# Kernel tuning notes

Hardware: AMD Instinct MI355X
Metric: run time of the kernel (lower is better)

The kernel has to match this reference:

```python
import jax, jax.numpy as jnp
import numpy as np

HEIGHT = 108
WIDTH = 108
LEN_CLASSES = 7
EPS = 1e-5


def layout_bbox(pred, H, W):
    # pred: [B, O, 4 + LEN_CLASSES]
    bbox = pred[..., :4]
    cls_prob = pred[..., 4:]  # [B,O,7]
    x_c = bbox[..., 0] * W   # [B,O]
    y_c = bbox[..., 1] * H
    w = bbox[..., 2] * W
    h = bbox[..., 3] * H
    x1 = (x_c - 0.5 * w)[:, :, None, None]  # [B,O,1,1]
    x2 = (x_c + 0.5 * w)[:, :, None, None]
    y1 = (y_c - 0.5 * h)[:, :, None, None]
    y2 = (y_c + 0.5 * h)[:, :, None, None]
    xt = jnp.arange(W, dtype=pred.dtype)[None, None, None, :]  # [1,1,1,W]
    yt = jnp.arange(H, dtype=pred.dtype)[None, None, :, None]  # [1,1,H,1]
    x1d = xt - x1  # [B,O,1,W]
    x2d = x2 - xt
    y1d = yt - y1  # [B,O,H,1]
    y2d = y2 - yt
    # min(relu(d), 1) == clip(d, 0, 1)
    yband = jnp.clip(y1d, 0.0, 1.0) * jnp.clip(y2d, 0.0, 1.0)  # [B,O,H,1]
    xband = jnp.clip(x1d, 0.0, 1.0) * jnp.clip(x2d, 0.0, 1.0)  # [B,O,1,W]
    x1_line = jax.nn.relu(1.0 - jnp.abs(x1d)) * yband  # [B,O,H,W]
    x2_line = jax.nn.relu(1.0 - jnp.abs(x2d)) * yband
    y1_line = jax.nn.relu(1.0 - jnp.abs(y1d)) * xband
    y2_line = jax.nn.relu(1.0 - jnp.abs(y2d)) * xband
    xy_max = jnp.maximum(jnp.maximum(x1_line, x2_line), jnp.maximum(y1_line, y2_line))  # [B,O,H,W]
    spatial = xy_max[..., None] * cls_prob[:, :, None, None, :]  # [B,O,H,W,7]
    return jnp.max(spatial, axis=1)  # [B,H,W,7]


def bn(x, g, b, axes):
    m = jnp.mean(x, axis=axes, keepdims=True)
    v = jnp.var(x, axis=axes, keepdims=True)
    shape = [1] * x.ndim
    shape[1 if x.ndim == 4 else -1] = -1
    return (x - m) * jax.lax.rsqrt(v + EPS) * g.reshape(shape) + b.reshape(shape)


def conv2d(x, w, b, stride):
    y = jax.lax.conv_general_dilated(x, w, (stride, stride), 'VALID',
                                     dimension_numbers=('NCHW', 'OIHW', 'NCHW'))
    return y + b[None, :, None, None]


def setup_inputs() -> dict:
    key = jax.random.key(0)
    ks = jax.random.split(key, 16)
    B, O = 64, 16
    d = {}
    d['image'] = jax.random.uniform(ks[0], (B, O, 4 + LEN_CLASSES), dtype=jnp.float32)
    d['conv1_w'] = jax.random.normal(ks[1], (32, LEN_CLASSES, 5, 5), jnp.float32) * 0.05
    d['conv1_b'] = jnp.zeros((32,), jnp.float32)
    d['bn1_g'] = jnp.ones((32,), jnp.float32)
    d['bn1_b'] = jnp.zeros((32,), jnp.float32)
    d['conv2_w'] = jax.random.normal(ks[2], (64, 32, 5, 5), jnp.float32) * 0.03
    d['conv2_b'] = jnp.zeros((64,), jnp.float32)
    d['bn2_g'] = jnp.ones((64,), jnp.float32)
    d['bn2_b'] = jnp.zeros((64,), jnp.float32)
    d['fc1_w'] = jax.random.normal(ks[3], (512, 36864), jnp.float32) * 0.005
    d['fc1_b'] = jnp.zeros((512,), jnp.float32)
    d['bn3_g'] = jnp.ones((512,), jnp.float32)
    d['bn3_b'] = jnp.zeros((512,), jnp.float32)
    d['fc2_w'] = jax.random.normal(ks[4], (1, 512), jnp.float32) * 0.04
    d['fc2_b'] = jnp.zeros((1,), jnp.float32)
    return d


def reference(image, conv1_w, conv1_b, bn1_g, bn1_b, conv2_w, conv2_b, bn2_g, bn2_b,
              fc1_w, fc1_b, bn3_g, bn3_b, fc2_w, fc2_b):
    # layout_bbox(image, WIDTH, HEIGHT): output_height=WIDTH, output_width=HEIGHT (both 108)
    layout = layout_bbox(image, WIDTH, HEIGHT)           # [B,108,108,7]
    x = jnp.transpose(layout, (0, 3, 1, 2))              # [B,7,108,108]
    x = conv2d(x, conv1_w, conv1_b, 2)                   # [B,32,52,52]
    x = bn(x, bn1_g, bn1_b, (0, 2, 3))
    x = jax.nn.leaky_relu(x, 0.2)
    x = conv2d(x, conv2_w, conv2_b, 2)                   # [B,64,24,24]
    x = bn(x, bn2_g, bn2_b, (0, 2, 3))
    x = jax.nn.leaky_relu(x, 0.2)
    x = x.reshape(x.shape[0], -1)                        # [B,36864]
    x = x @ fc1_w.T + fc1_b                              # [B,512]
    x = bn(x, bn3_g, bn3_b, (0,))
    x = jax.nn.leaky_relu(x, 0.2)
    x = x @ fc2_w.T + fc2_b                              # [B,1]
    return jax.nn.sigmoid(x)
```

## Files before the change

### kernel.cpp

```cpp
#include <hip/hip_runtime.h>
#include <hip/hip_bf16.h>


typedef unsigned short u16;
typedef __attribute__((ext_vector_type(8))) short bf8_t;
typedef __attribute__((ext_vector_type(4))) float f4_t;
#define MFMA16(a, b, c) __builtin_amdgcn_mfma_f32_16x16x32_bf16(a, b, c, 0, 0, 0)

#define LEAKY(v) (fmaxf((v), 0.2f * (v)))
#define CLIP01(v) fminf(fmaxf((v), 0.0f), 1.0f)

__device__ inline unsigned f2bf(float f) {
  unsigned u = __float_as_uint(f);
  return (u + 0x7FFFu + ((u >> 16) & 1u)) >> 16;
}
__device__ inline float bf2f(unsigned u) { return __uint_as_float(u << 16); }

constexpr int HW = 108;
constexpr int NOBJ = 16;
constexpr int NCLS = 7;

__global__ __launch_bounds__(128) void layout_prep_kernel(
    const float* __restrict__ image, const float* __restrict__ w1,
    const float* __restrict__ w2, u16* __restrict__ lay8,
    u16* __restrict__ wB1, u16* __restrict__ wB2, float* __restrict__ st) {
  int h = blockIdx.x, b = blockIdx.y;
  int tid = threadIdx.x;
  int bid = b * 108 + h;
  if (bid < 114) {
#pragma unroll
    for (int j = 0; j < 4; ++j) {
      int i = bid * 512 + j * 128 + tid;
      if (i < 1216) st[i] = 0.f;
      if (i < 7168) {
        int co = i / 224, k = i % 224;
        int chunk = k >> 5, kk = k & 31, tl = kk >> 3, ci = kk & 7;
        int tap = chunk * 4 + tl;
        unsigned v = 0;
        if (tap < 25 && ci < 7) v = f2bf(w1[co * 175 + ci * 25 + tap]);
        wB1[i] = (u16)v;
      } else if (i < 58368) {
        int jj = i - 7168;
        int tap = jj / 2048, r = jj % 2048, co = r >> 5, ci = r & 31;
        wB2[jj] = (u16)f2bf(w2[co * 800 + ci * 25 + tap]);
      }
    }
  }
  __shared__ float sIm[NOBJ * 11];
  for (int i = tid; i < NOBJ * 11; i += 128) sIm[i] = image[b * NOBJ * 11 + i];
  __syncthreads();
  int w = tid;
  if (w >= HW) return;
  float best[NCLS];
#pragma unroll
  for (int c = 0; c < NCLS; ++c) best[c] = 0.0f;
  float fw = (float)w, fh = (float)h;
  for (int o = 0; o < NOBJ; ++o) {
    const float* p = &sIm[o * 11];
    float xc = p[0] * 108.0f, yc = p[1] * 108.0f;
    float wd = p[2] * 108.0f, hd = p[3] * 108.0f;
    float x1 = xc - 0.5f * wd, x2 = xc + 0.5f * wd;
    float y1 = yc - 0.5f * hd, y2 = yc + 0.5f * hd;
    float x1d = fw - x1, x2d = x2 - fw;
    float y1d = fh - y1, y2d = y2 - fh;
    float yband = CLIP01(y1d) * CLIP01(y2d);
    float xband = CLIP01(x1d) * CLIP01(x2d);
    float x1l = fmaxf(1.0f - fabsf(x1d), 0.0f) * yband;
    float x2l = fmaxf(1.0f - fabsf(x2d), 0.0f) * yband;
    float y1l = fmaxf(1.0f - fabsf(y1d), 0.0f) * xband;
    float y2l = fmaxf(1.0f - fabsf(y2d), 0.0f) * xband;
    float xy = fmaxf(fmaxf(x1l, x2l), fmaxf(y1l, y2l));
#pragma unroll
    for (int c = 0; c < NCLS; ++c) best[c] = fmaxf(best[c], xy * p[4 + c]);
  }
  unsigned p0 = f2bf(best[0]) | (f2bf(best[1]) << 16);
  unsigned p1 = f2bf(best[2]) | (f2bf(best[3]) << 16);
  unsigned p2 = f2bf(best[4]) | (f2bf(best[5]) << 16);
  unsigned p3 = f2bf(best[6]);
  uint4 stv = {p0, p1, p2, p3};
  ((uint4*)lay8)[b * 11664 + h * 108 + w] = stv;
}

__global__ __launch_bounds__(128) void conv1_mfma(
    const u16* __restrict__ lay8, const u16* __restrict__ wB1,
    u16* __restrict__ x1r, float* __restrict__ bn1sum,
    float* __restrict__ bn1sq) {
  int mtg = blockIdx.x, nt = blockIdx.y, bz = blockIdx.z;
  int tid = threadIdx.x;
  int lane = tid & 63, wv = tid >> 6;
  int f = lane & 15, q = lane >> 4;
  int co = nt * 16 + f;
  int b0 = bz * 4 + wv * 2;
  int pbase[4];
  bool mvalid[4];
#pragma unroll
  for (int t = 0; t < 4; ++t) {
    int mt = mtg * 4 + t;
    mvalid[t] = mt < 169;
    int P = min(mt * 16 + f, 2703);
    int oh = P / 52, ow = P - oh * 52;
    pbase[t] = (oh * 2 * 108 + ow * 2) * 8;
  }
  f4_t acc[2][4];
#pragma unroll
  for (int b2 = 0; b2 < 2; ++b2)
#pragma unroll
    for (int t = 0; t < 4; ++t) acc[b2][t] = {0.f, 0.f, 0.f, 0.f};
#pragma unroll
  for (int chunk = 0; chunk < 7; ++chunk) {
    int tap = chunk * 4 + q;
    tap = tap > 24 ? 24 : tap;
    int kh = tap / 5, kw = tap - kh * 5;
    int toff = (kh * 108 + kw) * 8;
    bf8_t bf = *(const bf8_t*)&wB1[co * 224 + chunk * 32 + q * 8];
#pragma unroll
    for (int b2 = 0; b2 < 2; ++b2) {
      const u16* lb = lay8 + (size_t)(b0 + b2) * 93312;
#pragma unroll
      for (int t = 0; t < 4; ++t) {
        bf8_t af = *(const bf8_t*)&lb[pbase[t] + toff];
        acc[b2][t] = MFMA16(af, bf, acc[b2][t]);
      }
    }
  }
  float s = 0.f, sq = 0.f;
#pragma unroll
  for (int b2 = 0; b2 < 2; ++b2) {
    u16* ob = x1r + (size_t)(b0 + b2) * 86528;
#pragma unroll
    for (int t = 0; t < 4; ++t) {
      if (!mvalid[t]) continue;
      int P0 = (mtg * 4 + t) * 16 + q * 4;
#pragma unroll
      for (int r = 0; r < 4; ++r) {
        float v = acc[b2][t][r];
        s += v;
        sq += v * v;
        ob[(P0 + r) * 32 + co] = (u16)f2bf(v);
      }
    }
  }
  s += __shfl_xor(s, 16);
  s += __shfl_xor(s, 32);
  sq += __shfl_xor(sq, 16);
  sq += __shfl_xor(sq, 32);
  __shared__ float rs[2][16], rq[2][16];
  if (lane < 16) {
    rs[wv][f] = s;
    rq[wv][f] = sq;
  }
  __syncthreads();
  if (tid < 16) {
    atomicAdd(&bn1sum[nt * 16 + tid], rs[0][tid] + rs[1][tid]);
    atomicAdd(&bn1sq[nt * 16 + tid], rq[0][tid] + rq[1][tid]);
  }
}

__global__ __launch_bounds__(256) void bnapply1_kernel(
    const u16* __restrict__ x1r, const float* __restrict__ bn1sum,
    const float* __restrict__ bn1sq, const float* __restrict__ g1,
    const float* __restrict__ b1, u16* __restrict__ x1b) {
  int idx = blockIdx.x * 256 + threadIdx.x;
  int base = idx * 8, c0 = base & 31;
  float sc[8], sh[8];
#pragma unroll
  for (int j = 0; j < 8; ++j) {
    int c = c0 + j;
    float mean = bn1sum[c] * (1.f / 173056.f);
    float var = bn1sq[c] * (1.f / 173056.f) - mean * mean;
    float s = g1[c] * rsqrtf(var + 1e-5f);
    sc[j] = s;
    sh[j] = b1[c] - mean * s;
  }
  uint4 in = *(const uint4*)&x1r[base];
  unsigned w[4] = {in.x, in.y, in.z, in.w};
  unsigned out[4];
#pragma unroll
  for (int j = 0; j < 4; ++j) {
    float a = bf2f(w[j] & 0xffffu);
    float bq = bf2f(w[j] >> 16);
    a = LEAKY(fmaf(a, sc[2 * j], sh[2 * j]));
    bq = LEAKY(fmaf(bq, sc[2 * j + 1], sh[2 * j + 1]));
    out[j] = f2bf(a) | (f2bf(bq) << 16);
  }
  uint4 stv = {out[0], out[1], out[2], out[3]};
  *(uint4*)&x1b[base] = stv;
}

__global__ __launch_bounds__(256) void conv2_mfma(
    const u16* __restrict__ x1b, const u16* __restrict__ wB2,
    u16* __restrict__ x2b, float* __restrict__ bn2sum,
    float* __restrict__ bn2sq) {
  int mt = blockIdx.x, ntg = blockIdx.y, bz = blockIdx.z;
  int tid = threadIdx.x;
  int lane = tid & 63, wv = tid >> 6;
  int f = lane & 15, q = lane >> 4;
  int co0 = ntg * 32;
  int b0 = bz * 16 + wv * 4;
  int P = mt * 16 + f;
  int oh = P / 24, ow = P - oh * 24;
  int abase = (oh * 2 * 52 + ow * 2) * 32 + q * 8;
  f4_t acc[4][2];
#pragma unroll
  for (int b2 = 0; b2 < 4; ++b2)
#pragma unroll
    for (int n = 0; n < 2; ++n) acc[b2][n] = {0.f, 0.f, 0.f, 0.f};
#pragma unroll
  for (int tap = 0; tap < 25; ++tap) {
    int kh = tap / 5, kw = tap - kh * 5;
    int toff = (kh * 52 + kw) * 32;
    bf8_t bf0 = *(const bf8_t*)&wB2[tap * 2048 + (co0 + f) * 32 + q * 8];
    bf8_t bf1 = *(const bf8_t*)&wB2[tap * 2048 + (co0 + 16 + f) * 32 + q * 8];
#pragma unroll
    for (int b2 = 0; b2 < 4; ++b2) {
      bf8_t af =
          *(const bf8_t*)&x1b[(size_t)(b0 + b2) * 86528 + abase + toff];
      acc[b2][0] = MFMA16(af, bf0, acc[b2][0]);
      acc[b2][1] = MFMA16(af, bf1, acc[b2][1]);
    }
  }
  float s[2] = {0.f, 0.f}, sq[2] = {0.f, 0.f};
#pragma unroll
  for (int b2 = 0; b2 < 4; ++b2) {
    u16* ob = x2b + (size_t)(b0 + b2) * 36864;
#pragma unroll
    for (int n = 0; n < 2; ++n)
#pragma unroll
      for (int r = 0; r < 4; ++r) {
        float v = acc[b2][n][r];
        s[n] += v;
        sq[n] += v * v;
        ob[(mt * 16 + q * 4 + r) * 64 + co0 + n * 16 + f] = (u16)f2bf(v);
      }
  }
#pragma unroll
  for (int n = 0; n < 2; ++n) {
    s[n] += __shfl_xor(s[n], 16);
    s[n] += __shfl_xor(s[n], 32);
    sq[n] += __shfl_xor(sq[n], 16);
    sq[n] += __shfl_xor(sq[n], 32);
  }
  __shared__ float rs[4][32], rq[4][32];
  if (lane < 16) {
#pragma unroll
    for (int n = 0; n < 2; ++n) {
      rs[wv][n * 16 + f] = s[n];
      rq[wv][n * 16 + f] = sq[n];
    }
  }
  __syncthreads();
  if (tid < 32) {
    atomicAdd(&bn2sum[co0 + tid],
              rs[0][tid] + rs[1][tid] + rs[2][tid] + rs[3][tid]);
    atomicAdd(&bn2sq[co0 + tid],
              rq[0][tid] + rq[1][tid] + rq[2][tid] + rq[3][tid]);
  }
}

__global__ __launch_bounds__(256) void bnapply2t_kernel(
    const u16* __restrict__ x2b, const float* __restrict__ bn2sum,
    const float* __restrict__ bn2sq, const float* __restrict__ g2,
    const float* __restrict__ b2, u16* __restrict__ xB) {
  int hw0 = blockIdx.x * 64, b = blockIdx.y;
  __shared__ float tile[64 * 65];
  int t = threadIdx.x;
  int c = t & 63, hl4 = t >> 6;
  float mean = bn2sum[c] * (1.f / 36864.f);
  float var = bn2sq[c] * (1.f / 36864.f) - mean * mean;
  float s = g2[c] * rsqrtf(var + 1e-5f);
  float h = b2[c] - mean * s;
#pragma unroll
  for (int it = 0; it < 16; ++it) {
    int hl = it * 4 + hl4;
    float v = bf2f((unsigned)x2b[((size_t)b * 576 + hw0 + hl) * 64 + c]);
    tile[hl * 65 + c] = LEAKY(fmaf(v, s, h));
  }
  __syncthreads();
  int hw = t & 63, cl4 = t >> 6;
#pragma unroll
  for (int it = 0; it < 16; ++it) {
    int cc = it * 4 + cl4;
    xB[(size_t)b * 36864 + cc * 576 + hw0 + hw] = (u16)f2bf(tile[hw * 65 + cc]);
  }
}

__global__ __launch_bounds__(256) void fc1_mfma(
    const u16* __restrict__ xB, const float* __restrict__ wgt,
    float* __restrict__ part) {
  int ks = blockIdx.x, nb = blockIdx.y;
  int tid = threadIdx.x;
  int lane = tid & 63, wv = tid >> 6;
  int f = lane & 15, q = lane >> 4;
  int n0 = nb * 64 + wv * 16;
  int kbase = ks * 512;
  __shared__ u16 sA[64 * 520];
#pragma unroll
  for (int i = 0; i < 16; ++i) {
    int c = i * 256 + tid;
    int row = c >> 6, col = c & 63;
    *(uint4*)&sA[row * 520 + col * 8] =
        *(const uint4*)&xB[(size_t)row * 36864 + kbase + col * 8];
  }
  __syncthreads();
  f4_t acc[4];
#pragma unroll
  for (int m = 0; m < 4; ++m) acc[m] = {0.f, 0.f, 0.f, 0.f};
  const float* wrow = wgt + (size_t)(n0 + f) * 36864 + kbase + q * 8;
#pragma unroll 4
  for (int kt = 0; kt < 16; ++kt) {
    const float* wp = wrow + kt * 32;
    float4 wa = *(const float4*)wp;
    float4 wb = *(const float4*)(wp + 4);
    union { bf8_t v; u16 u[8]; } bu;
    bu.u[0] = (u16)f2bf(wa.x); bu.u[1] = (u16)f2bf(wa.y);
    bu.u[2] = (u16)f2bf(wa.z); bu.u[3] = (u16)f2bf(wa.w);
    bu.u[4] = (u16)f2bf(wb.x); bu.u[5] = (u16)f2bf(wb.y);
    bu.u[6] = (u16)f2bf(wb.z); bu.u[7] = (u16)f2bf(wb.w);
    bf8_t afr[4];
#pragma unroll
    for (int m = 0; m < 4; ++m)
      afr[m] = *(const bf8_t*)&sA[(m * 16 + f) * 520 + kt * 32 + q * 8];
#pragma unroll
    for (int m = 0; m < 4; ++m) acc[m] = MFMA16(afr[m], bu.v, acc[m]);
  }
  float* pp = part + (size_t)ks * 32768;
#pragma unroll
  for (int m = 0; m < 4; ++m)
#pragma unroll
    for (int r = 0; r < 4; ++r)
      pp[(m * 16 + q * 4 + r) * 512 + n0 + f] = acc[m][r];
}

__global__ __launch_bounds__(256) void fc1_reduce_kernel(
    const float* __restrict__ part, float* __restrict__ fc1o,
    float* __restrict__ bn3sum, float* __restrict__ bn3sq) {
  int i = blockIdx.x * 256 + threadIdx.x;
  float s = 0.f;
#pragma unroll 8
  for (int ks = 0; ks < 72; ++ks) s += part[(size_t)ks * 32768 + i];
  fc1o[i] = s;
  atomicAdd(&bn3sum[i & 511], s);
  atomicAdd(&bn3sq[i & 511], s * s);
}

__global__ __launch_bounds__(64) void fc2_kernel(
    const float* __restrict__ fc1o, const float* __restrict__ bn3sum,
    const float* __restrict__ bn3sq, const float* __restrict__ g3,
    const float* __restrict__ b3, const float* __restrict__ w2,
    const float* __restrict__ b2o, float* __restrict__ out) {
  int m = blockIdx.x;
  int fl = threadIdx.x;
  float a = 0.f;
#pragma unroll
  for (int j = 0; j < 8; ++j) {
    int ff = fl + j * 64;
    float mean = bn3sum[ff] * (1.f / 64.f);
    float var = bn3sq[ff] * (1.f / 64.f) - mean * mean;
    float sc = g3[ff] * rsqrtf(var + 1e-5f);
    float sh = b3[ff] - mean * sc;
    float v = LEAKY(fmaf(fc1o[m * 512 + ff], sc, sh));
    a += v * w2[ff];
  }
  for (int off = 32; off; off >>= 1) a += __shfl_down(a, off, 64);
  if (fl == 0) out[m] = 1.f / (1.f + expf(-(a + b2o[0])));
}

extern "C" void kernel_launch(void* const* d_in, const int* in_sizes, int n_in,
                              void* d_out, int out_size, void* d_ws,
                              size_t ws_size, hipStream_t stream) {
  const float* image = (const float*)d_in[0];
  const float* c1w = (const float*)d_in[1];
  const float* bn1g = (const float*)d_in[3];
  const float* bn1b = (const float*)d_in[4];
  const float* c2w = (const float*)d_in[5];
  const float* bn2g = (const float*)d_in[7];
  const float* bn2b = (const float*)d_in[8];
  const float* f1w = (const float*)d_in[9];
  const float* bn3g = (const float*)d_in[11];
  const float* bn3b = (const float*)d_in[12];
  const float* f2w = (const float*)d_in[13];
  const float* f2b = (const float*)d_in[14];
  float* ws = (float*)d_ws;

  u16* lay8 = (u16*)ws;
  u16* x1r = (u16*)(ws + 2985984);
  u16* x1b = (u16*)(ws + 5754880);
  u16* x2b = (u16*)(ws + 8523776);
  u16* xB = (u16*)(ws + 9703424);
  float* fc1part = ws + 10883072;
  float* fc1o = ws + 13242368;
  float* st = ws + 13275136;
  float* bn1sum = st, *bn1sq = st + 32;
  float* bn2sum = st + 64, *bn2sq = st + 128;
  float* bn3sum = st + 192, *bn3sq = st + 704;
  u16* wB1 = (u16*)(ws + 13276352);
  u16* wB2 = (u16*)(ws + 13279936);

  layout_prep_kernel<<<dim3(108, 64), 128, 0, stream>>>(image, c1w, c2w, lay8,
                                                        wB1, wB2, st);
  conv1_mfma<<<dim3(43, 2, 16), 128, 0, stream>>>(lay8, wB1, x1r, bn1sum,
                                                  bn1sq);
  bnapply1_kernel<<<2704, 256, 0, stream>>>(x1r, bn1sum, bn1sq, bn1g, bn1b,
                                            x1b);
  conv2_mfma<<<dim3(36, 2, 4), 256, 0, stream>>>(x1b, wB2, x2b, bn2sum,
                                                 bn2sq);
  bnapply2t_kernel<<<dim3(9, 64), 256, 0, stream>>>(x2b, bn2sum, bn2sq, bn2g,
                                                    bn2b, xB);
  fc1_mfma<<<dim3(72, 8), 256, 0, stream>>>(xB, f1w, fc1part);
  fc1_reduce_kernel<<<128, 256, 0, stream>>>(fc1part, fc1o, bn3sum, bn3sq);
  fc2_kernel<<<64, 64, 0, stream>>>(fc1o, bn3sum, bn3sq, bn3g, bn3b, f2w, f2b,
                                    (float*)d_out);
}
```

Baseline: 239.4 us.

## Retile conv1 per batch over all channels; halve conv2 batch tile and reduce block size

conv1 now has each wave cover one batch image and all 32 output channels, so each A fragment loaded from the layout feeds two MFMAs instead of being reloaded for the second channel tile. The grid becomes 43x32 blocks instead of 43x2x16. conv2 processes 2 batches per wave instead of 4, which doubles the grid to raise occupancy at the cost of less weight reuse. fc1_reduce uses 128-thread blocks with twice as many blocks, spreading the work across more CUs.

```diff
diff --git a/kernel.cpp b/kernel.cpp
--- a/kernel.cpp
+++ b/kernel.cpp
@@ -85,12 +85,11 @@
     const u16* __restrict__ lay8, const u16* __restrict__ wB1,
     u16* __restrict__ x1r, float* __restrict__ bn1sum,
     float* __restrict__ bn1sq) {
-  int mtg = blockIdx.x, nt = blockIdx.y, bz = blockIdx.z;
+  int mtg = blockIdx.x, bg = blockIdx.y;
   int tid = threadIdx.x;
   int lane = tid & 63, wv = tid >> 6;
   int f = lane & 15, q = lane >> 4;
-  int co = nt * 16 + f;
-  int b0 = bz * 4 + wv * 2;
+  int b = bg * 2 + wv;
   int pbase[4];
   bool mvalid[4];
 #pragma unroll
@@ -103,56 +102,60 @@
   }
   f4_t acc[2][4];
 #pragma unroll
-  for (int b2 = 0; b2 < 2; ++b2)
-#pragma unroll
-    for (int t = 0; t < 4; ++t) acc[b2][t] = {0.f, 0.f, 0.f, 0.f};
+  for (int nt = 0; nt < 2; ++nt)
+#pragma unroll
+    for (int t = 0; t < 4; ++t) acc[nt][t] = {0.f, 0.f, 0.f, 0.f};
+  const u16* lb = lay8 + (size_t)b * 93312;
 #pragma unroll
   for (int chunk = 0; chunk < 7; ++chunk) {
     int tap = chunk * 4 + q;
     tap = tap > 24 ? 24 : tap;
     int kh = tap / 5, kw = tap - kh * 5;
     int toff = (kh * 108 + kw) * 8;
-    bf8_t bf = *(const bf8_t*)&wB1[co * 224 + chunk * 32 + q * 8];
-#pragma unroll
-    for (int b2 = 0; b2 < 2; ++b2) {
-      const u16* lb = lay8 + (size_t)(b0 + b2) * 93312;
-#pragma unroll
-      for (int t = 0; t < 4; ++t) {
-        bf8_t af = *(const bf8_t*)&lb[pbase[t] + toff];
-        acc[b2][t] = MFMA16(af, bf, acc[b2][t]);
+    bf8_t bf0 = *(const bf8_t*)&wB1[f * 224 + chunk * 32 + q * 8];
+    bf8_t bf1 = *(const bf8_t*)&wB1[(16 + f) * 224 + chunk * 32 + q * 8];
+#pragma unroll
+    for (int t = 0; t < 4; ++t) {
+      bf8_t af = *(const bf8_t*)&lb[pbase[t] + toff];
+      acc[0][t] = MFMA16(af, bf0, acc[0][t]);
+      acc[1][t] = MFMA16(af, bf1, acc[1][t]);
+    }
+  }
+  float s[2] = {0.f, 0.f}, sq[2] = {0.f, 0.f};
+  u16* ob = x1r + (size_t)b * 86528;
+#pragma unroll
+  for (int t = 0; t < 4; ++t) {
+    if (!mvalid[t]) continue;
+    int P0 = (mtg * 4 + t) * 16 + q * 4;
+#pragma unroll
+    for (int nt = 0; nt < 2; ++nt)
+#pragma unroll
+      for (int r = 0; r < 4; ++r) {
+        float v = acc[nt][t][r];
+        s[nt] += v;
+        sq[nt] += v * v;
+        ob[(P0 + r) * 32 + nt * 16 + f] = (u16)f2bf(v);
       }
+  }
+#pragma unroll
+  for (int nt = 0; nt < 2; ++nt) {
+    s[nt] += __shfl_xor(s[nt], 16);
+    s[nt] += __shfl_xor(s[nt], 32);
+    sq[nt] += __shfl_xor(sq[nt], 16);
+    sq[nt] += __shfl_xor(sq[nt], 32);
+  }
+  __shared__ float rs[2][32], rq[2][32];
+  if (lane < 16) {
+#pragma unroll
+    for (int nt = 0; nt < 2; ++nt) {
+      rs[wv][nt * 16 + f] = s[nt];
+      rq[wv][nt * 16 + f] = sq[nt];
     }
   }
-  float s = 0.f, sq = 0.f;
-#pragma unroll
-  for (int b2 = 0; b2 < 2; ++b2) {
-    u16* ob = x1r + (size_t)(b0 + b2) * 86528;
-#pragma unroll
-    for (int t = 0; t < 4; ++t) {
-      if (!mvalid[t]) continue;
-      int P0 = (mtg * 4 + t) * 16 + q * 4;
-#pragma unroll
-      for (int r = 0; r < 4; ++r) {
-        float v = acc[b2][t][r];
-        s += v;
-        sq += v * v;
-        ob[(P0 + r) * 32 + co] = (u16)f2bf(v);
-      }
-    }
-  }
-  s += __shfl_xor(s, 16);
-  s += __shfl_xor(s, 32);
-  sq += __shfl_xor(sq, 16);
-  sq += __shfl_xor(sq, 32);
-  __shared__ float rs[2][16], rq[2][16];
-  if (lane < 16) {
-    rs[wv][f] = s;
-    rq[wv][f] = sq;
-  }
   __syncthreads();
-  if (tid < 16) {
-    atomicAdd(&bn1sum[nt * 16 + tid], rs[0][tid] + rs[1][tid]);
-    atomicAdd(&bn1sq[nt * 16 + tid], rq[0][tid] + rq[1][tid]);
+  if (tid < 32) {
+    atomicAdd(&bn1sum[tid], rs[0][tid] + rs[1][tid]);
+    atomicAdd(&bn1sq[tid], rq[0][tid] + rq[1][tid]);
   }
 }
 
@@ -196,13 +199,13 @@
   int lane = tid & 63, wv = tid >> 6;
   int f = lane & 15, q = lane >> 4;
   int co0 = ntg * 32;
-  int b0 = bz * 16 + wv * 4;
+  int b0 = bz * 8 + wv * 2;
   int P = mt * 16 + f;
   int oh = P / 24, ow = P - oh * 24;
   int abase = (oh * 2 * 52 + ow * 2) * 32 + q * 8;
-  f4_t acc[4][2];
-#pragma unroll
-  for (int b2 = 0; b2 < 4; ++b2)
+  f4_t acc[2][2];
+#pragma unroll
+  for (int b2 = 0; b2 < 2; ++b2)
 #pragma unroll
     for (int n = 0; n < 2; ++n) acc[b2][n] = {0.f, 0.f, 0.f, 0.f};
 #pragma unroll
@@ -212,7 +215,7 @@
     bf8_t bf0 = *(const bf8_t*)&wB2[tap * 2048 + (co0 + f) * 32 + q * 8];
     bf8_t bf1 = *(const bf8_t*)&wB2[tap * 2048 + (co0 + 16 + f) * 32 + q * 8];
 #pragma unroll
-    for (int b2 = 0; b2 < 4; ++b2) {
+    for (int b2 = 0; b2 < 2; ++b2) {
       bf8_t af =
           *(const bf8_t*)&x1b[(size_t)(b0 + b2) * 86528 + abase + toff];
       acc[b2][0] = MFMA16(af, bf0, acc[b2][0]);
@@ -221,7 +224,7 @@
   }
   float s[2] = {0.f, 0.f}, sq[2] = {0.f, 0.f};
 #pragma unroll
-  for (int b2 = 0; b2 < 4; ++b2) {
+  for (int b2 = 0; b2 < 2; ++b2) {
     u16* ob = x2b + (size_t)(b0 + b2) * 36864;
 #pragma unroll
     for (int n = 0; n < 2; ++n)
@@ -331,10 +334,10 @@
       pp[(m * 16 + q * 4 + r) * 512 + n0 + f] = acc[m][r];
 }
 
-__global__ __launch_bounds__(256) void fc1_reduce_kernel(
+__global__ __launch_bounds__(128) void fc1_reduce_kernel(
     const float* __restrict__ part, float* __restrict__ fc1o,
     float* __restrict__ bn3sum, float* __restrict__ bn3sq) {
-  int i = blockIdx.x * 256 + threadIdx.x;
+  int i = blockIdx.x * 128 + threadIdx.x;
   float s = 0.f;
 #pragma unroll 8
   for (int ks = 0; ks < 72; ++ks) s += part[(size_t)ks * 32768 + i];
@@ -398,16 +401,15 @@
 
   layout_prep_kernel<<<dim3(108, 64), 128, 0, stream>>>(image, c1w, c2w, lay8,
                                                         wB1, wB2, st);
-  conv1_mfma<<<dim3(43, 2, 16), 128, 0, stream>>>(lay8, wB1, x1r, bn1sum,
-                                                  bn1sq);
+  conv1_mfma<<<dim3(43, 32), 128, 0, stream>>>(lay8, wB1, x1r, bn1sum, bn1sq);
   bnapply1_kernel<<<2704, 256, 0, stream>>>(x1r, bn1sum, bn1sq, bn1g, bn1b,
                                             x1b);
-  conv2_mfma<<<dim3(36, 2, 4), 256, 0, stream>>>(x1b, wB2, x2b, bn2sum,
+  conv2_mfma<<<dim3(36, 2, 8), 256, 0, stream>>>(x1b, wB2, x2b, bn2sum,
                                                  bn2sq);
   bnapply2t_kernel<<<dim3(9, 64), 256, 0, stream>>>(x2b, bn2sum, bn2sq, bn2g,
                                                     bn2b, xB);
   fc1_mfma<<<dim3(72, 8), 256, 0, stream>>>(xB, f1w, fc1part);
-  fc1_reduce_kernel<<<128, 256, 0, stream>>>(fc1part, fc1o, bn3sum, bn3sq);
+  fc1_reduce_kernel<<<256, 128, 0, stream>>>(fc1part, fc1o, bn3sum, bn3sq);
   fc2_kernel<<<64, 64, 0, stream>>>(fc1o, bn3sum, bn3sq, bn3g, bn3b, f2w, f2b,
                                     (float*)d_out);
 }
```

Result: slower. 253.9 us (+6.1%).

## Fuse BN1 apply and leaky ReLU into conv2 via LDS-staged input rows

Applied to the files above, without the earlier changes.

Removes the separate bnapply1 kernel. conv2 now loads the raw conv1 output rows for one batch and a 16-pixel output tile into shared memory, applies BN1 scale/shift and leaky ReLU during staging, then runs MFMA taps from LDS. The grid becomes per-batch and per-tile, with each wave handling 16 output channels. This saves one kernel launch and a full write plus read of the intermediate activation. In exchange, overlapping input rows are re-normalized redundantly across neighbouring tiles, and each block issues more atomics for the BN2 statistics.

```diff
diff --git a/kernel.cpp b/kernel.cpp
--- a/kernel.cpp
+++ b/kernel.cpp
@@ -156,104 +156,91 @@
   }
 }
 
-__global__ __launch_bounds__(256) void bnapply1_kernel(
-    const u16* __restrict__ x1r, const float* __restrict__ bn1sum,
-    const float* __restrict__ bn1sq, const float* __restrict__ g1,
-    const float* __restrict__ b1, u16* __restrict__ x1b) {
-  int idx = blockIdx.x * 256 + threadIdx.x;
-  int base = idx * 8, c0 = base & 31;
-  float sc[8], sh[8];
-#pragma unroll
-  for (int j = 0; j < 8; ++j) {
-    int c = c0 + j;
-    float mean = bn1sum[c] * (1.f / 173056.f);
-    float var = bn1sq[c] * (1.f / 173056.f) - mean * mean;
-    float s = g1[c] * rsqrtf(var + 1e-5f);
-    sc[j] = s;
-    sh[j] = b1[c] - mean * s;
-  }
-  uint4 in = *(const uint4*)&x1r[base];
-  unsigned w[4] = {in.x, in.y, in.z, in.w};
-  unsigned out[4];
-#pragma unroll
-  for (int j = 0; j < 4; ++j) {
-    float a = bf2f(w[j] & 0xffffu);
-    float bq = bf2f(w[j] >> 16);
-    a = LEAKY(fmaf(a, sc[2 * j], sh[2 * j]));
-    bq = LEAKY(fmaf(bq, sc[2 * j + 1], sh[2 * j + 1]));
-    out[j] = f2bf(a) | (f2bf(bq) << 16);
-  }
-  uint4 stv = {out[0], out[1], out[2], out[3]};
-  *(uint4*)&x1b[base] = stv;
-}
-
-__global__ __launch_bounds__(256) void conv2_mfma(
-    const u16* __restrict__ x1b, const u16* __restrict__ wB2,
+__global__ __launch_bounds__(256) void conv2_lds(
+    const u16* __restrict__ x1r, const u16* __restrict__ wB2,
+    const float* __restrict__ bn1sum, const float* __restrict__ bn1sq,
+    const float* __restrict__ g1, const float* __restrict__ b1,
     u16* __restrict__ x2b, float* __restrict__ bn2sum,
     float* __restrict__ bn2sq) {
-  int mt = blockIdx.x, ntg = blockIdx.y, bz = blockIdx.z;
+  int mt = blockIdx.x, b = blockIdx.y;
   int tid = threadIdx.x;
   int lane = tid & 63, wv = tid >> 6;
   int f = lane & 15, q = lane >> 4;
-  int co0 = ntg * 32;
-  int b0 = bz * 16 + wv * 4;
+  __shared__ u16 sA[7 * 52 * 32];
+  __shared__ float rsm[64], rqm[64];
+  int oh0 = (mt * 16) / 24;
+  int base = 2 * oh0;
+  {
+    float sc1[8], sh1[8];
+    int oc = (tid & 3) * 8;
+#pragma unroll
+    for (int j = 0; j < 8; ++j) {
+      int c = oc + j;
+      float mean = bn1sum[c] * (1.f / 173056.f);
+      float var = bn1sq[c] * (1.f / 173056.f) - mean * mean;
+      float s = g1[c] * rsqrtf(var + 1e-5f);
+      sc1[j] = s;
+      sh1[j] = b1[c] - mean * s;
+    }
+    const u16* xb = x1r + (size_t)b * 86528;
+#pragma unroll
+    for (int it = 0; it < 6; ++it) {
+      int ci = it * 256 + tid;
+      if (ci < 1456) {
+        int r = ci / 208, k = ci - r * 208;
+        int gr = base + r;
+        gr = gr > 51 ? 51 : gr;
+        uint4 raw = *(const uint4*)&xb[gr * 1664 + k * 8];
+        unsigned wd[4] = {raw.x, raw.y, raw.z, raw.w};
+        unsigned out[4];
+#pragma unroll
+        for (int k2 = 0; k2 < 4; ++k2) {
+          float lo = bf2f(wd[k2] & 0xffffu);
+          float hi = bf2f(wd[k2] >> 16);
+          lo = LEAKY(fmaf(lo, sc1[2 * k2], sh1[2 * k2]));
+          hi = LEAKY(fmaf(hi, sc1[2 * k2 + 1], sh1[2 * k2 + 1]));
+          out[k2] = f2bf(lo) | (f2bf(hi) << 16);
+        }
+        uint4 stv = {out[0], out[1], out[2], out[3]};
+        *(uint4*)&sA[r * 1664 + k * 8] = stv;
+      }
+    }
+  }
+  __syncthreads();
   int P = mt * 16 + f;
   int oh = P / 24, ow = P - oh * 24;
-  int abase = (oh * 2 * 52 + ow * 2) * 32 + q * 8;
-  f4_t acc[4][2];
-#pragma unroll
-  for (int b2 = 0; b2 < 4; ++b2)
-#pragma unroll
-    for (int n = 0; n < 2; ++n) acc[b2][n] = {0.f, 0.f, 0.f, 0.f};
+  int drow = 2 * oh - base;
+  int co = wv * 16 + f;
+  f4_t acc = {0.f, 0.f, 0.f, 0.f};
 #pragma unroll
   for (int tap = 0; tap < 25; ++tap) {
     int kh = tap / 5, kw = tap - kh * 5;
-    int toff = (kh * 52 + kw) * 32;
-    bf8_t bf0 = *(const bf8_t*)&wB2[tap * 2048 + (co0 + f) * 32 + q * 8];
-    bf8_t bf1 = *(const bf8_t*)&wB2[tap * 2048 + (co0 + 16 + f) * 32 + q * 8];
-#pragma unroll
-    for (int b2 = 0; b2 < 4; ++b2) {
-      bf8_t af =
-          *(const bf8_t*)&x1b[(size_t)(b0 + b2) * 86528 + abase + toff];
-      acc[b2][0] = MFMA16(af, bf0, acc[b2][0]);
-      acc[b2][1] = MFMA16(af, bf1, acc[b2][1]);
-    }
-  }
-  float s[2] = {0.f, 0.f}, sq[2] = {0.f, 0.f};
-#pragma unroll
-  for (int b2 = 0; b2 < 4; ++b2) {
-    u16* ob = x2b + (size_t)(b0 + b2) * 36864;
-#pragma unroll
-    for (int n = 0; n < 2; ++n)
-#pragma unroll
-      for (int r = 0; r < 4; ++r) {
-        float v = acc[b2][n][r];
-        s[n] += v;
-        sq[n] += v * v;
-        ob[(mt * 16 + q * 4 + r) * 64 + co0 + n * 16 + f] = (u16)f2bf(v);
-      }
-  }
-#pragma unroll
-  for (int n = 0; n < 2; ++n) {
-    s[n] += __shfl_xor(s[n], 16);
-    s[n] += __shfl_xor(s[n], 32);
-    sq[n] += __shfl_xor(sq[n], 16);
-    sq[n] += __shfl_xor(sq[n], 32);
-  }
-  __shared__ float rs[4][32], rq[4][32];
+    bf8_t af =
+        *(const bf8_t*)&sA[(drow + kh) * 1664 + (2 * ow + kw) * 32 + q * 8];
+    bf8_t bf = *(const bf8_t*)&wB2[tap * 2048 + co * 32 + q * 8];
+    acc = MFMA16(af, bf, acc);
+  }
+  u16* ob = x2b + (size_t)b * 36864;
+  float s = 0.f, sq = 0.f;
+#pragma unroll
+  for (int rr = 0; rr < 4; ++rr) {
+    float v = acc[rr];
+    s += v;
+    sq += v * v;
+    ob[(mt * 16 + q * 4 + rr) * 64 + co] = (u16)f2bf(v);
+  }
+  s += __shfl_xor(s, 16);
+  s += __shfl_xor(s, 32);
+  sq += __shfl_xor(sq, 16);
+  sq += __shfl_xor(sq, 32);
   if (lane < 16) {
-#pragma unroll
-    for (int n = 0; n < 2; ++n) {
-      rs[wv][n * 16 + f] = s[n];
-      rq[wv][n * 16 + f] = sq[n];
-    }
-  }
-  __syncthreads();
-  if (tid < 32) {
-    atomicAdd(&bn2sum[co0 + tid],
-              rs[0][tid] + rs[1][tid] + rs[2][tid] + rs[3][tid]);
-    atomicAdd(&bn2sq[co0 + tid],
-              rq[0][tid] + rq[1][tid] + rq[2][tid] + rq[3][tid]);
+    rsm[wv * 16 + lane] = s;
+    rqm[wv * 16 + lane] = sq;
+  }
+  __syncthreads();
+  if (tid < 64) {
+    atomicAdd(&bn2sum[tid], rsm[tid]);
+    atomicAdd(&bn2sq[tid], rqm[tid]);
   }
 }
 
@@ -384,7 +371,6 @@
 
   u16* lay8 = (u16*)ws;
   u16* x1r = (u16*)(ws + 2985984);
-  u16* x1b = (u16*)(ws + 5754880);
   u16* x2b = (u16*)(ws + 8523776);
   u16* xB = (u16*)(ws + 9703424);
   float* fc1part = ws + 10883072;
@@ -400,10 +386,8 @@
                                                         wB1, wB2, st);
   conv1_mfma<<<dim3(43, 2, 16), 128, 0, stream>>>(lay8, wB1, x1r, bn1sum,
                                                   bn1sq);
-  bnapply1_kernel<<<2704, 256, 0, stream>>>(x1r, bn1sum, bn1sq, bn1g, bn1b,
-                                            x1b);
-  conv2_mfma<<<dim3(36, 2, 4), 256, 0, stream>>>(x1b, wB2, x2b, bn2sum,
-                                                 bn2sq);
+  conv2_lds<<<dim3(36, 64), 256, 0, stream>>>(x1r, wB2, bn1sum, bn1sq, bn1g,
+                                              bn1b, x2b, bn2sum, bn2sq);
   bnapply2t_kernel<<<dim3(9, 64), 256, 0, stream>>>(x2b, bn2sum, bn2sq, bn2g,
                                                     bn2b, xB);
   fc1_mfma<<<dim3(72, 8), 256, 0, stream>>>(xB, f1w, fc1part);
```

Result: slower. 262.4 us (+9.6%).
